# Kernel optimization log

Hardware: AMD Instinct MI355X
Metric: run time of the kernel (lower is better)

Reference implementation:

```python
import jax, jax.numpy as jnp
import numpy as np

N, E, B = 50000, 800000, 512
DIN, H, A, BT = 128, 256, 40, 5


def _ln(h, g, b):
    m = jnp.mean(h, -1, keepdims=True)
    v = jnp.mean((h - m) ** 2, -1, keepdims=True)
    return (h - m) * jax.lax.rsqrt(v + 1e-5) * g + b


def _gcn(x, w, b, src, dst, n):
    # PyG GCNConv: add self-loops, symmetric D^-1/2 (A+I) D^-1/2 normalization
    h = x @ w
    loop = jnp.arange(n)
    s = jnp.concatenate([src, loop])
    d = jnp.concatenate([dst, loop])
    deg = jax.ops.segment_sum(jnp.ones(s.shape[0], h.dtype), d, num_segments=n)
    dinv = jax.lax.rsqrt(jnp.maximum(deg, 1.0))
    coef = (dinv[s] * dinv[d])[:, None]
    return jax.ops.segment_sum(coef * h[s], d, num_segments=n) + b


def _mlp2(x, w1, b1, w2, b2):
    return jax.nn.relu(x @ w1 + b1) @ w2 + b2


def _mlp3(x, w1, b1, w2, b2, w3, b3):
    h = jax.nn.relu(x @ w1 + b1)
    h = jax.nn.relu(h @ w2 + b2)
    return h @ w3 + b3


def setup_inputs() -> dict:
    key = jax.random.key(0)
    ks = iter(jax.random.split(key, 64))
    p = lambda shape: jax.random.normal(next(ks), shape, jnp.float32) * 0.05
    inp = {}
    inp["x"] = jax.random.normal(next(ks), (N, DIN), jnp.float32)
    inp["edge_index"] = jax.random.randint(next(ks), (2, E), 0, N)
    inp["batch"] = jnp.sort(jax.random.randint(next(ks), (N,), 0, B))
    inp["new_node_indices"] = jax.random.randint(next(ks), (B,), 0, N)
    inp["focus_node_indices"] = jax.random.randint(next(ks), (B,), 0, N)
    inp["num_graphs"] = B
    inp["conv_w0"] = p((DIN, H)); inp["conv_b0"] = p((H,))
    inp["conv_w1"] = p((H, H)); inp["conv_b1"] = p((H,))
    inp["conv_w2"] = p((H, H)); inp["conv_b2"] = p((H,))
    for i in range(3):
        inp[f"ln_g{i}"] = jnp.ones((H,), jnp.float32)
        inp[f"ln_b{i}"] = jnp.zeros((H,), jnp.float32)
    inp["res_w0"] = p((DIN, H)); inp["res_b0"] = p((H,))
    inp["stop_w1"] = p((H, H)); inp["stop_b1"] = p((H,))
    inp["stop_w2"] = p((H, 1)); inp["stop_b2"] = p((1,))
    inp["addn_w1"] = p((H, H)); inp["addn_b1"] = p((H,))
    inp["addn_w2"] = p((H, A)); inp["addn_b2"] = p((A,))
    inp["addb_w1"] = p((H, H)); inp["addb_b1"] = p((H,))
    inp["addb_w2"] = p((H, BT)); inp["addb_b2"] = p((BT,))
    inp["edge_w1"] = p((2 * H, H)); inp["edge_b1"] = p((H,))
    inp["edge_w2"] = p((H, H // 2)); inp["edge_b2"] = p((H // 2,))
    inp["edge_w3"] = p((H // 2, 1)); inp["edge_b3"] = p((1,))
    inp["bond_w1"] = p((2 * H, H)); inp["bond_b1"] = p((H,))
    inp["bond_w2"] = p((H, H // 2)); inp["bond_b2"] = p((H // 2,))
    inp["bond_w3"] = p((H // 2, BT)); inp["bond_b3"] = p((BT,))
    return inp


def reference(x, edge_index, batch, new_node_indices, focus_node_indices, num_graphs,
              conv_w0, conv_b0, conv_w1, conv_b1, conv_w2, conv_b2,
              ln_g0, ln_b0, ln_g1, ln_b1, ln_g2, ln_b2,
              res_w0, res_b0,
              stop_w1, stop_b1, stop_w2, stop_b2,
              addn_w1, addn_b1, addn_w2, addn_b2,
              addb_w1, addb_b1, addb_w2, addb_b2,
              edge_w1, edge_b1, edge_w2, edge_b2, edge_w3, edge_b3,
              bond_w1, bond_b1, bond_w2, bond_b2, bond_w3, bond_b3):
    n = x.shape[0]
    src, dst = edge_index[0], edge_index[1]
    conv_params = [(conv_w0, conv_b0), (conv_w1, conv_b1), (conv_w2, conv_b2)]
    ln_params = [(ln_g0, ln_b0), (ln_g1, ln_b1), (ln_g2, ln_b2)]
    h = x
    for i in range(3):
        h_in = h
        cw, cb = conv_params[i]
        lg, lb = ln_params[i]
        h = _gcn(h, cw, cb, src, dst, n)
        h = jax.nn.relu(_ln(h, lg, lb))  # dropout: eval mode (identity)
        res = h_in @ res_w0 + res_b0 if i == 0 else h_in
        h = h + res
    node_embeddings = h  # [N, H]
    # global mean pool over graphs
    counts = jax.ops.segment_sum(jnp.ones(n, h.dtype), batch, num_segments=num_graphs)
    graph_embedding = jax.ops.segment_sum(node_embeddings, batch, num_segments=num_graphs) / jnp.maximum(counts, 1.0)[:, None]
    stop_logits = _mlp2(graph_embedding, stop_w1, stop_b1, stop_w2, stop_b2)
    add_node_logits = _mlp2(graph_embedding, addn_w1, addn_b1, addn_w2, addn_b2)
    add_bond_logits = _mlp2(node_embeddings[focus_node_indices], addb_w1, addb_b1, addb_w2, addb_b2)
    # pair each node with its graph's newly added node
    new_node_embeddings = node_embeddings[new_node_indices]  # [B, H]
    pair = jnp.concatenate([node_embeddings, new_node_embeddings[batch]], axis=1)  # [N, 2H]
    edge_selection_logits = _mlp3(pair, edge_w1, edge_b1, edge_w2, edge_b2, edge_w3, edge_b3)
    bond_type_logits = _mlp3(pair, bond_w1, bond_b1, bond_w2, bond_b2, bond_w3, bond_b3)
    return (stop_logits, add_node_logits, add_bond_logits, node_embeddings,
            edge_selection_logits, bond_type_logits)
```

## Files before the change

### kernel.cpp

```cpp
#include <hip/hip_runtime.h>

typedef short bf16x8 __attribute__((ext_vector_type(8)));
typedef float f32x4 __attribute__((ext_vector_type(4)));
typedef unsigned short u16;
typedef u16 u16x8 __attribute__((ext_vector_type(8)));

__device__ __forceinline__ float bf2f(u16 u) {
  union { float f; unsigned int i; } x; x.i = ((unsigned int)u) << 16; return x.f;
}
__device__ __forceinline__ u16 f2bf(float f) {
  union { float f; unsigned int i; } x; x.f = f;
  unsigned int r = x.i + 0x7fffu + ((x.i >> 16) & 1u);
  return (u16)(r >> 16);
}
__device__ __forceinline__ void st_out_(void* out, size_t idx, float v, int f32) {
  if (f32) ((float*)out)[idx] = v;
  else ((u16*)out)[idx] = f2bf(v);
}

__global__ void k_detect(const u16* __restrict__ xx, int* flag) {
  int j = threadIdx.x;
  u16 u = xx[2 * j];
  int ex = (u >> 7) & 0xFF;
  int insane = (u != 0) && (ex < 100 || ex > 140);
  unsigned long long m = __ballot(insane);
  if (j == 0) flag[0] = (__popcll(m) > 8) ? 1 : 0;
}

__global__ void k_cvt_big(const void* __restrict__ src, u16* __restrict__ dst, int n,
                          const int* __restrict__ flag) {
  int i = blockIdx.x * 256 + threadIdx.x;
  if (i >= n) return;
  dst[i] = (*flag) ? f2bf(((const float*)src)[i]) : ((const u16*)src)[i];
}

#define NSEG 38
struct Cvt { const void* src[NSEG]; int off[NSEG + 1]; };
__global__ void k_cvt_all(Cvt c, u16* __restrict__ dst, int total, const int* __restrict__ flag) {
  int i = blockIdx.x * 256 + threadIdx.x;
  if (i >= total) return;
  int s = 0;
  #pragma unroll 1
  while (i >= c.off[s + 1]) s++;
  int j = i - c.off[s];
  dst[i] = (*flag) ? f2bf(((const float*)c.src[s])[j]) : ((const u16*)c.src[s])[j];
}

__global__ void k_padbias(const u16* __restrict__ rb, u16* cbz) {
  int i = blockIdx.x * 256 + threadIdx.x;
  if (i < 512) cbz[i] = (i < 256) ? (u16)0 : rb[i - 256];
}

struct Tr { const u16* src[8]; u16* dst[8]; int lk[8]; int nc[8]; int off[9]; };
__global__ void k_tr_all(Tr c, int total) {
  int i = blockIdx.x * 256 + threadIdx.x;
  if (i >= total) return;
  int s = 0;
  #pragma unroll 1
  while (i >= c.off[s + 1]) s++;
  int j = i - c.off[s];
  int K = 1 << c.lk[s];
  int nrow = j >> c.lk[s], k = j & (K - 1);
  c.dst[s][j] = c.src[s][k * c.nc[s] + nrow];
}

__global__ void k_init(int* deg, int* cursor, int n) {
  int i = blockIdx.x * 256 + threadIdx.x;
  if (i < n) { deg[i] = 1; cursor[i] = 0; }
}
__global__ void k_deg(const int* __restrict__ dst, int* deg, int e) {
  int i = blockIdx.x * 256 + threadIdx.x;
  if (i < e) atomicAdd(&deg[dst[i]], 1);
}
__global__ void k_dinv(const int* __restrict__ deg, float* dinv, int n) {
  int i = blockIdx.x * 256 + threadIdx.x;
  if (i < n) dinv[i] = rsqrtf((float)deg[i]);
}
#define SCB 4096
__global__ __launch_bounds__(256) void k_scanA(const int* __restrict__ deg, int* bsum, int n) {
  int b = blockIdx.x, t = threadIdx.x;
  int base = b * SCB;
  int s = 0;
  for (int j = t; j < SCB; j += 256) { int i = base + j; s += (i < n) ? deg[i] - 1 : 0; }
  int l = t & 63, wid = t >> 6;
  #pragma unroll
  for (int o = 32; o; o >>= 1) s += __shfl_xor(s, o);
  __shared__ int red[4];
  if (l == 0) red[wid] = s;
  __syncthreads();
  if (t == 0) bsum[b] = red[0] + red[1] + red[2] + red[3];
}
__global__ void k_scanB(int* bsum, int nb, int* off, int n) {
  if (threadIdx.x == 0) {
    int c = 0;
    for (int i = 0; i < nb; i++) { int v = bsum[i]; bsum[i] = c; c += v; }
    off[n] = c;
  }
}
__global__ __launch_bounds__(256) void k_scanC(const int* __restrict__ deg, const int* __restrict__ bsum,
                                               int* off, int n) {
  int b = blockIdx.x, t = threadIdx.x;
  int base = b * SCB + t * 16;
  int loc[16]; int s = 0;
  #pragma unroll
  for (int j = 0; j < 16; j++) { int i = base + j; loc[j] = s; s += (i < n) ? deg[i] - 1 : 0; }
  int l = t & 63, wid = t >> 6;
  int incl = s;
  #pragma unroll
  for (int o = 1; o < 64; o <<= 1) { int y = __shfl_up(incl, o); if (l >= o) incl += y; }
  int excl = incl - s;
  __shared__ int ws[4];
  if (l == 63) ws[wid] = incl;
  __syncthreads();
  int woff = 0;
  for (int w = 0; w < wid; w++) woff += ws[w];
  int pre = bsum[b] + woff + excl;
  #pragma unroll
  for (int j = 0; j < 16; j++) { int i = base + j; if (i < n) off[i] = pre + loc[j]; }
}
__global__ void k_csr(const int* __restrict__ src, const int* __restrict__ dst,
                      const int* __restrict__ off, int* cursor, int* csr_src, int e) {
  int i = blockIdx.x * 256 + threadIdx.x;
  if (i >= e) return;
  int d = dst[i], s = src[i];
  int slot = atomicAdd(&cursor[d], 1);
  csr_src[off[d] + slot] = s;
}

template <int EPI, int K>
__global__ __launch_bounds__(512) void gemm_p(
    const u16* __restrict__ A, int lda,
    const u16* __restrict__ Bt,
    u16* __restrict__ C, int ldc,
    int M, int NC,
    const u16* __restrict__ colbias,
    const float* __restrict__ rowbias, int rbld, const int* __restrict__ rowmap) {
  __shared__ u16 Bs[64 * K];
  __shared__ u16 As[8 * 4 * 512];
  const int t = threadIdx.x;
  const int n0 = blockIdx.x * 64;
  const int m0 = blockIdx.y * 512;
  {
    const int ng = K >> 3;
    const int tot = 64 * ng;
    for (int i = t; i < tot; i += 512) {
      int c = i / ng, g = i - c * ng;
      u16x8 v = *reinterpret_cast<const u16x8*>(Bt + (size_t)(n0 + c) * K + g * 8);
      *reinterpret_cast<u16x8*>(&Bs[c * K + (g ^ (c & 7)) * 8]) = v;
    }
  }
  __syncthreads();

  const int wid = t >> 6, l = t & 63;
  const int rbase = m0 + wid * 64;
  const int lr = l & 15, lg = l >> 4;
  u16* Aw = &As[wid * 2048];
  const int srow = l >> 2;
  const int sg = (l & 3) ^ (srow & 3);

  auto stage = [&](int s) {
    int mi = s & 3, kk = s >> 2;
    int row = rbase + mi * 16 + srow;
    if (row >= M) row = M - 1;
    __builtin_amdgcn_global_load_lds(
        (const __attribute__((address_space(1))) unsigned int*)(A + (size_t)row * lda + kk * 32 + sg * 8),
        (__attribute__((address_space(3))) unsigned int*)(Aw + (s & 3) * 512), 16, 0, 0);
  };

  f32x4 acc[4][4] = {};
  bf16x8 bfr[4];
  const int S = K >> 3;
  stage(0); stage(1); stage(2);
  #pragma unroll
  for (int s = 0; s < S; s++) {
    const int buf = s & 3, mi = s & 3, kk = s >> 2;
    __builtin_amdgcn_sched_barrier(0);
    if (s + 3 < S) stage(s + 3);
    const int rem = (s + 3 < S) ? 3 : (S - 1 - s);
    if (rem >= 3)      asm volatile("s_waitcnt vmcnt(3)" ::: "memory");
    else if (rem == 2) asm volatile("s_waitcnt vmcnt(2)" ::: "memory");
    else if (rem == 1) asm volatile("s_waitcnt vmcnt(1)" ::: "memory");
    else               asm volatile("s_waitcnt vmcnt(0)" ::: "memory");
    __builtin_amdgcn_sched_barrier(0);
    if (mi == 0) {
      #pragma unroll
      for (int ni = 0; ni < 4; ni++) {
        int g = kk * 4 + lg;
        bfr[ni] = *reinterpret_cast<const bf16x8*>(&Bs[(ni * 16 + lr) * K + (g ^ (lr & 7)) * 8]);
      }
    }
    const u16* Ab = Aw + buf * 512;
    bf16x8 af = *reinterpret_cast<const bf16x8*>(&Ab[lr * 32 + (lg ^ (lr & 3)) * 8]);
    #pragma unroll
    for (int ni = 0; ni < 4; ni++)
      acc[mi][ni] = __builtin_amdgcn_mfma_f32_16x16x32_bf16(af, bfr[ni], acc[mi][ni], 0, 0, 0);
  }

  #pragma unroll
  for (int mi = 0; mi < 4; mi++) {
    int rowi[4];
    #pragma unroll
    for (int r = 0; r < 4; r++) rowi[r] = rbase + mi * 16 + lg * 4 + r;
    float rbv[4][4];
    if (EPI == 3) {
      int rmv[4];
      #pragma unroll
      for (int r = 0; r < 4; r++) {
        int rr = rowi[r]; if (rr >= M) rr = M - 1;
        rmv[r] = rowmap[rr];
      }
      #pragma unroll
      for (int ni = 0; ni < 4; ni++)
        #pragma unroll
        for (int r = 0; r < 4; r++)
          rbv[ni][r] = rowbias[(size_t)rmv[r] * rbld + n0 + ni * 16 + lr];
    }
    #pragma unroll
    for (int ni = 0; ni < 4; ni++) {
      int col = n0 + ni * 16 + lr;
      float cbv = 0.f;
      if (EPI == 1 || EPI == 2) cbv = bf2f(colbias[col]);
      #pragma unroll
      for (int r = 0; r < 4; r++) {
        if (rowi[r] < M) {
          float v = acc[mi][ni][r];
          if (EPI == 1 || EPI == 2) v += cbv;
          if (EPI == 3) v += rbv[ni][r];
          if (EPI == 2 || EPI == 3) v = fmaxf(v, 0.f);
          C[(size_t)rowi[r] * ldc + col] = f2bf(v);
        }
      }
    }
  }
}

__global__ __launch_bounds__(256, 6) void k_agg(
    const u16* __restrict__ hw, int hwld, const u16* __restrict__ cb,
    const u16* __restrict__ lng, const u16* __restrict__ lnb,
    const u16* __restrict__ res, int resld, const float* __restrict__ dinv,
    const int* __restrict__ off, const int* __restrict__ csr_src,
    u16* __restrict__ hout, int n) {
  int l = threadIdx.x & 63;
  int v = blockIdx.x * 4 + (threadIdx.x >> 6);
  if (v >= n) return;
  const int half = l >> 5;
  const int c0 = (l & 31) * 8;
  float a[8] = {0, 0, 0, 0, 0, 0, 0, 0};
  int s = off[v], e = off[v + 1];
  int i = s;
  for (; i + 7 < e; i += 8) {
    int u0 = csr_src[i + half],     u1 = csr_src[i + 2 + half];
    int u2 = csr_src[i + 4 + half], u3 = csr_src[i + 6 + half];
    float w0 = dinv[u0], w1 = dinv[u1], w2 = dinv[u2], w3 = dinv[u3];
    u16x8 r0 = *reinterpret_cast<const u16x8*>(hw + (size_t)u0 * hwld + c0);
    u16x8 r1 = *reinterpret_cast<const u16x8*>(hw + (size_t)u1 * hwld + c0);
    u16x8 r2 = *reinterpret_cast<const u16x8*>(hw + (size_t)u2 * hwld + c0);
    u16x8 r3 = *reinterpret_cast<const u16x8*>(hw + (size_t)u3 * hwld + c0);
    #pragma unroll
    for (int j = 0; j < 8; j++)
      a[j] += w0 * bf2f(r0[j]) + w1 * bf2f(r1[j]) + w2 * bf2f(r2[j]) + w3 * bf2f(r3[j]);
  }
  for (; i < e; i += 2) {
    int idx = i + half;
    if (idx < e) {
      int u = csr_src[idx];
      float w = dinv[u];
      u16x8 r = *reinterpret_cast<const u16x8*>(hw + (size_t)u * hwld + c0);
      #pragma unroll
      for (int j = 0; j < 8; j++) a[j] += w * bf2f(r[j]);
    }
  }
  #pragma unroll
  for (int j = 0; j < 8; j++) a[j] += __shfl_xor(a[j], 32);
  float dv = dinv[v];
  u16x8 sv = *reinterpret_cast<const u16x8*>(hw + (size_t)v * hwld + c0);
  u16x8 cbv = *reinterpret_cast<const u16x8*>(cb + c0);
  float sum = 0.f;
  #pragma unroll
  for (int j = 0; j < 8; j++) {
    a[j] = dv * (dv * bf2f(sv[j]) + a[j]) + bf2f(cbv[j]);
    sum += a[j];
  }
  #pragma unroll
  for (int o = 16; o; o >>= 1) sum += __shfl_xor(sum, o);
  float mean = sum * (1.f / 256.f);
  float vs = 0.f;
  #pragma unroll
  for (int j = 0; j < 8; j++) { float d = a[j] - mean; vs += d * d; }
  #pragma unroll
  for (int o = 16; o; o >>= 1) vs += __shfl_xor(vs, o);
  float rs = rsqrtf(vs * (1.f / 256.f) + 1e-5f);
  u16x8 gv = *reinterpret_cast<const u16x8*>(lng + c0);
  u16x8 bv = *reinterpret_cast<const u16x8*>(lnb + c0);
  u16x8 rv = *reinterpret_cast<const u16x8*>(res + (size_t)v * resld + c0);
  u16x8 ov;
  #pragma unroll
  for (int j = 0; j < 8; j++)
    ov[j] = f2bf(fmaxf((a[j] - mean) * rs * bf2f(gv[j]) + bf2f(bv[j]), 0.f) + bf2f(rv[j]));
  if (half == 0)
    *reinterpret_cast<u16x8*>(hout + (size_t)v * 256 + c0) = ov;
}

__global__ __launch_bounds__(256) void k_pool(const u16* __restrict__ h, const int* __restrict__ batch,
                                              int n, float* gemb) {
  int g = blockIdx.x, c = threadIdx.x;
  int lo = 0, hi = n;
  while (lo < hi) { int mid = (lo + hi) >> 1; if (batch[mid] < g) lo = mid + 1; else hi = mid; }
  int s = lo;
  lo = s; hi = n;
  while (lo < hi) { int mid = (lo + hi) >> 1; if (batch[mid] < g + 1) lo = mid + 1; else hi = mid; }
  int e = lo;
  float a0 = 0.f, a1 = 0.f, a2 = 0.f, a3 = 0.f;
  int i = s;
  for (; i + 3 < e; i += 4) {
    a0 += bf2f(h[(size_t)i * 256 + c]);
    a1 += bf2f(h[(size_t)(i + 1) * 256 + c]);
    a2 += bf2f(h[(size_t)(i + 2) * 256 + c]);
    a3 += bf2f(h[(size_t)(i + 3) * 256 + c]);
  }
  for (; i < e; i++) a0 += bf2f(h[(size_t)i * 256 + c]);
  float acc = (a0 + a1) + (a2 + a3);
  int cnt = e - s; if (cnt < 1) cnt = 1;
  gemb[g * 256 + c] = acc / (float)cnt;
}

__global__ __launch_bounds__(256) void k_glin(const u16* __restrict__ h, const int* __restrict__ nidx,
                                              const u16* __restrict__ W, const u16* __restrict__ b1,
                                              float* g1, int ld, int ofs) {
  int b = blockIdx.x, t = threadIdx.x;
  __shared__ float sin_[256];
  sin_[t] = bf2f(h[(size_t)nidx[b] * 256 + t]);
  __syncthreads();
  float acc = bf2f(b1[t]);
  #pragma unroll 8
  for (int k = 0; k < 256; k++) acc += sin_[k] * bf2f(W[k * 256 + t]);
  g1[(size_t)b * ld + ofs + t] = acc;
}

template <int OUTD>
__global__ __launch_bounds__(256) void k_mlp2(const float* __restrict__ inf32,
                                              const u16* __restrict__ inbf, const int* __restrict__ idx,
                                              const u16* __restrict__ W1, const u16* __restrict__ b1,
                                              const u16* __restrict__ W2, const u16* __restrict__ b2,
                                              void* __restrict__ out, size_t obase,
                                              const int* __restrict__ flag) {
  int b = blockIdx.x, t = threadIdx.x;
  __shared__ float sin_[256];
  __shared__ float sh[256];
  sin_[t] = inf32 ? inf32[b * 256 + t] : bf2f(inbf[(size_t)idx[b] * 256 + t]);
  __syncthreads();
  float acc = bf2f(b1[t]);
  #pragma unroll 8
  for (int k = 0; k < 256; k++) acc += sin_[k] * bf2f(W1[k * 256 + t]);
  sh[t] = fmaxf(acc, 0.f);
  __syncthreads();
  if (t < OUTD) {
    float a2 = bf2f(b2[t]);
    #pragma unroll 8
    for (int k = 0; k < 256; k++) a2 += sh[k] * bf2f(W2[k * OUTD + t]);
    st_out_(out, obase + (size_t)b * OUTD + t, a2, *flag);
  }
}

__global__ __launch_bounds__(256) void k_final(const u16* __restrict__ t2e, const u16* __restrict__ t2b,
                                               const u16* __restrict__ w3e, const u16* __restrict__ b3e,
                                               const u16* __restrict__ w3b, const u16* __restrict__ b3b,
                                               void* __restrict__ out, size_t oe, size_t ob, int M,
                                               const int* __restrict__ flag) {
  int r = blockIdx.x * 4 + (threadIdx.x >> 6);
  int l = threadIdx.x & 63;
  if (r >= M) return;
  float p[6] = {0, 0, 0, 0, 0, 0};
  #pragma unroll
  for (int j = 0; j < 2; j++) {
    int k = l * 2 + j;
    float te = bf2f(t2e[(size_t)r * 128 + k]);
    float tb = bf2f(t2b[(size_t)r * 128 + k]);
    p[0] += te * bf2f(w3e[k]);
    #pragma unroll
    for (int q = 0; q < 5; q++) p[1 + q] += tb * bf2f(w3b[k * 5 + q]);
  }
  #pragma unroll
  for (int q = 0; q < 6; q++)
    #pragma unroll
    for (int o = 32; o; o >>= 1) p[q] += __shfl_xor(p[q], o);
  if (l == 0) {
    int f32 = *flag;
    st_out_(out, oe + r, p[0] + bf2f(b3e[0]), f32);
    #pragma unroll
    for (int q = 0; q < 5; q++)
      st_out_(out, ob + (size_t)r * 5 + q, p[1 + q] + bf2f(b3b[q]), f32);
  }
}

__global__ void k_emit8(const u16* __restrict__ src, void* __restrict__ out, size_t obase, int n8,
                        const int* __restrict__ flag) {
  int i = blockIdx.x * 256 + threadIdx.x;
  if (i >= n8) return;
  u16x8 v = reinterpret_cast<const u16x8*>(src)[i];
  if (*flag) {
    float4* fo = (float4*)((float*)out + obase);
    float4 lo, hi;
    lo.x = bf2f(v[0]); lo.y = bf2f(v[1]); lo.z = bf2f(v[2]); lo.w = bf2f(v[3]);
    hi.x = bf2f(v[4]); hi.y = bf2f(v[5]); hi.z = bf2f(v[6]); hi.w = bf2f(v[7]);
    fo[(size_t)i * 2] = lo; fo[(size_t)i * 2 + 1] = hi;
  } else {
    reinterpret_cast<u16x8*>((u16*)out + obase)[i] = v;
  }
}

extern "C" void kernel_launch(void* const* d_in, const int* in_sizes, int n_in,
                              void* d_out, int out_size, void* d_ws, size_t ws_size,
                              hipStream_t stream) {
  const int N = in_sizes[0] / 128;
  const int E = in_sizes[1] / 2;
  const int B = in_sizes[3];

  const int* ei    = (const int*)d_in[1];
  const int* srcp  = ei;
  const int* dstp  = ei + E;
  const int* batch = (const int*)d_in[2];
  const int* newi  = (const int*)d_in[3];
  const int* focus = (const int*)d_in[4];

  const size_t o_stop = 0;
  const size_t o_addn = (size_t)B;
  const size_t o_addb = (size_t)B + (size_t)B * 40;
  const size_t o_emb  = o_addb + (size_t)B * 5;
  const size_t o_esel = o_emb + (size_t)N * 256;
  const size_t o_bond = o_esel + (size_t)N;

  char* p = (char*)d_ws;
  auto alloc = [&](size_t bytes) -> void* {
    void* r = (void*)p;
    p += (bytes + 255) & ~(size_t)255;
    return r;
  };
  int* flag = (int*)alloc(4);
  static const int seg_din[NSEG] = {6,7,8,9,10,11, 12,13,14,15,16,17, 18,19,
                                    20,21,22,23, 24,25,26,27, 28,29,30,31,
                                    32,33,34,35,36,37, 38,39,40,41,42,43};
  static const int seg_len[NSEG] = {32768,256,65536,256,65536,256, 256,256,256,256,256,256,
                                    32768,256, 65536,256,256,1, 65536,256,10240,40,
                                    65536,256,1280,5, 131072,256,32768,128,128,1,
                                    131072,256,32768,128,640,5};
  int wtotal = 0;
  int seg_off[NSEG + 1];
  for (int i = 0; i < NSEG; i++) { seg_off[i] = wtotal; wtotal += seg_len[i]; }
  seg_off[NSEG] = wtotal;
  u16* wbf = (u16*)alloc((size_t)wtotal * 2);
  u16* wt_f0  = (u16*)alloc(512 * 128 * 2);
  u16* wt_cw1 = (u16*)alloc(256 * 256 * 2);
  u16* wt_cw2 = (u16*)alloc(256 * 256 * 2);
  u16* wt_t1  = (u16*)alloc(512 * 256 * 2);
  u16* wt_e2  = (u16*)alloc(128 * 256 * 2);
  u16* wt_b2  = (u16*)alloc(128 * 256 * 2);
  u16* cbz    = (u16*)alloc(512 * 2);
  int*   deg     = (int*)alloc((size_t)N * 4);
  int*   cursor  = (int*)alloc((size_t)N * 4);
  int*   off     = (int*)alloc((size_t)(N + 1) * 4);
  float* dinv    = (float*)alloc((size_t)N * 4);
  int*   bsum    = (int*)alloc(64 * 4);
  float* gemb    = (float*)alloc((size_t)B * 256 * 4);
  float* g1full  = (float*)alloc((size_t)B * 512 * 4);
  int*   csr_src = (int*)alloc((size_t)E * 4);
  u16*   xbf     = (u16*)alloc((size_t)N * 128 * 2);
  u16*   P1      = (u16*)alloc((size_t)N * 256 * 2);
  u16*   P2      = (u16*)alloc((size_t)N * 256 * 2);
  u16*   P3      = (u16*)alloc((size_t)N * 256 * 2);

  auto wseg = [&](int i) -> u16* { return wbf + seg_off[i]; };
  u16 *cw0 = wseg(0), *cb0 = wseg(1), *cw1 = wseg(2), *cb1 = wseg(3), *cw2 = wseg(4), *cb2 = wseg(5);
  u16 *lg0 = wseg(6), *lb0 = wseg(7), *lg1 = wseg(8), *lb1 = wseg(9), *lg2 = wseg(10), *lb2 = wseg(11);
  u16 *rw0 = wseg(12), *rb0 = wseg(13);
  u16 *sw1 = wseg(14), *sb1 = wseg(15), *sw2 = wseg(16), *sb2 = wseg(17);
  u16 *aw1 = wseg(18), *ab1 = wseg(19), *aw2 = wseg(20), *ab2 = wseg(21);
  u16 *bw1 = wseg(22), *bb1 = wseg(23), *bw2 = wseg(24), *bb2 = wseg(25);
  u16 *ew1 = wseg(26), *eb1 = wseg(27), *ew2 = wseg(28), *eb2 = wseg(29), *ew3 = wseg(30), *eb3 = wseg(31);
  u16 *qw1 = wseg(32), *qb1 = wseg(33), *qw2 = wseg(34), *qb2 = wseg(35), *qw3 = wseg(36), *qb3 = wseg(37);

  k_detect<<<1, 64, 0, stream>>>((const u16*)d_in[0], flag);
  k_cvt_big<<<(N * 128 + 255) / 256, 256, 0, stream>>>(d_in[0], xbf, N * 128, flag);
  Cvt cd;
  for (int i = 0; i < NSEG; i++) cd.src[i] = d_in[seg_din[i]];
  for (int i = 0; i <= NSEG; i++) cd.off[i] = seg_off[i];
  k_cvt_all<<<(wtotal + 255) / 256, 256, 0, stream>>>(cd, wbf, wtotal, flag);
  k_padbias<<<2, 256, 0, stream>>>(rb0, cbz);

  const int NB = (N + 255) / 256;
  const int EBk = (E + 255) / 256;
  const int NBS = (N + SCB - 1) / SCB;

  k_init<<<NB, 256, 0, stream>>>(deg, cursor, N);
  k_deg<<<EBk, 256, 0, stream>>>(dstp, deg, E);
  k_dinv<<<NB, 256, 0, stream>>>(deg, dinv, N);
  k_scanA<<<NBS, 256, 0, stream>>>(deg, bsum, N);
  k_scanB<<<1, 64, 0, stream>>>(bsum, NBS, off, N);
  k_scanC<<<NBS, 256, 0, stream>>>(deg, bsum, off, N);
  k_csr<<<EBk, 256, 0, stream>>>(srcp, dstp, off, cursor, csr_src, E);

  {
    Tr td;
    const u16* ts[8] = {cw0, rw0, cw1, cw2, ew1, qw1, ew2, qw2};
    u16* tdst[8] = {wt_f0, wt_f0 + 256 * 128, wt_cw1, wt_cw2, wt_t1, wt_t1 + 256 * 256, wt_e2, wt_b2};
    int tlk[8] = {7, 7, 8, 8, 8, 8, 8, 8};
    int tnc[8] = {256, 256, 256, 256, 256, 256, 128, 128};
    int tlen[8] = {32768, 32768, 65536, 65536, 65536, 65536, 32768, 32768};
    int tot = 0;
    for (int i = 0; i < 8; i++) {
      td.src[i] = ts[i]; td.dst[i] = tdst[i]; td.lk[i] = tlk[i]; td.nc[i] = tnc[i];
      td.off[i] = tot; tot += tlen[i];
    }
    td.off[8] = tot;
    k_tr_all<<<(tot + 255) / 256, 256, 0, stream>>>(td, tot);
  }

  const int MB5 = (N + 511) / 512;
  const int AGB = (N + 3) / 4;
  u16* PF = P1;

  gemm_p<1, 128><<<dim3(8, MB5), 512, 0, stream>>>(xbf, 128, wt_f0, PF, 512, N, 512, cbz, nullptr, 0, nullptr);
  k_agg<<<AGB, 256, 0, stream>>>(PF, 512, cb0, lg0, lb0, PF + 256, 512, dinv, off, csr_src, P3, N);
  gemm_p<0, 256><<<dim3(4, MB5), 512, 0, stream>>>(P3, 256, wt_cw1, P1, 256, N, 256, nullptr, nullptr, 0, nullptr);
  k_agg<<<AGB, 256, 0, stream>>>(P1, 256, cb1, lg1, lb1, P3, 256, dinv, off, csr_src, P2, N);
  gemm_p<0, 256><<<dim3(4, MB5), 512, 0, stream>>>(P2, 256, wt_cw2, P1, 256, N, 256, nullptr, nullptr, 0, nullptr);
  k_agg<<<AGB, 256, 0, stream>>>(P1, 256, cb2, lg2, lb2, P2, 256, dinv, off, csr_src, P3, N);

  k_emit8<<<(N * 256 / 8 + 255) / 256, 256, 0, stream>>>(P3, d_out, o_emb, N * 256 / 8, flag);

  k_pool<<<B, 256, 0, stream>>>(P3, batch, N, gemb);
  k_glin<<<B, 256, 0, stream>>>(P3, newi, ew1 + 256 * 256, eb1, g1full, 512, 0);
  k_glin<<<B, 256, 0, stream>>>(P3, newi, qw1 + 256 * 256, qb1, g1full, 512, 256);
  k_mlp2<1><<<B, 256, 0, stream>>>(gemb, nullptr, nullptr, sw1, sb1, sw2, sb2, d_out, o_stop, flag);
  k_mlp2<40><<<B, 256, 0, stream>>>(gemb, nullptr, nullptr, aw1, ab1, aw2, ab2, d_out, o_addn, flag);
  k_mlp2<5><<<B, 256, 0, stream>>>(nullptr, P3, focus, bw1, bb1, bw2, bb2, d_out, o_addb, flag);

  u16* T1 = PF;
  gemm_p<3, 256><<<dim3(8, MB5), 512, 0, stream>>>(P3, 256, wt_t1, T1, 512, N, 512, nullptr, g1full, 512, batch);
  u16* t2e = P3;
  u16* t2b = P3 + (size_t)N * 128;
  gemm_p<2, 256><<<dim3(2, MB5), 512, 0, stream>>>(T1, 512, wt_e2, t2e, 128, N, 128, eb2, nullptr, 0, nullptr);
  gemm_p<2, 256><<<dim3(2, MB5), 512, 0, stream>>>(T1 + 256, 512, wt_b2, t2b, 128, N, 128, qb2, nullptr, 0, nullptr);
  k_final<<<(N + 3) / 4, 256, 0, stream>>>(t2e, t2b, ew3, eb3, qw3, qb3, d_out, o_esel, o_bond, N, flag);
}
```

Before: 615.2 us.

## Precompute edge weights in CSR, fuse embedding emit, swap GEMM grid order

The CSR build now stores dinv[src] per edge, so aggregation reads a contiguous weight array instead of doing a dependent random gather into dinv. The final aggregation kernel writes the node embeddings straight to the output buffer, which removes the separate k_emit8 pass over N×256 values. GEMM launches now put M tiles on grid x, padded to a multiple of 8 with an early-exit guard, likely for better L2 reuse or XCD distribution of the shared B tiles. k_agg launch bounds are raised to allow more waves per SIMD. The cost is an extra E-sized float array plus its write, and possible register pressure in k_agg.

```diff
diff --git a/kernel.cpp b/kernel.cpp
--- a/kernel.cpp
+++ b/kernel.cpp
@@ -119,12 +119,15 @@
   for (int j = 0; j < 16; j++) { int i = base + j; if (i < n) off[i] = pre + loc[j]; }
 }
 __global__ void k_csr(const int* __restrict__ src, const int* __restrict__ dst,
-                      const int* __restrict__ off, int* cursor, int* csr_src, int e) {
+                      const float* __restrict__ dinv, const int* __restrict__ off,
+                      int* cursor, int* csr_src, float* csr_w, int e) {
   int i = blockIdx.x * 256 + threadIdx.x;
   if (i >= e) return;
   int d = dst[i], s = src[i];
   int slot = atomicAdd(&cursor[d], 1);
-  csr_src[off[d] + slot] = s;
+  int pos = off[d] + slot;
+  csr_src[pos] = s;
+  csr_w[pos] = dinv[s];
 }
 
 template <int EPI, int K>
@@ -138,8 +141,9 @@
   __shared__ u16 Bs[64 * K];
   __shared__ u16 As[8 * 4 * 512];
   const int t = threadIdx.x;
-  const int n0 = blockIdx.x * 64;
-  const int m0 = blockIdx.y * 512;
+  const int m0 = blockIdx.x * 512;
+  const int n0 = blockIdx.y * 64;
+  if (m0 >= M) return;
   {
     const int ng = K >> 3;
     const int tot = 64 * ng;
@@ -234,12 +238,14 @@
   }
 }
 
-__global__ __launch_bounds__(256, 6) void k_agg(
+__global__ __launch_bounds__(256, 8) void k_agg(
     const u16* __restrict__ hw, int hwld, const u16* __restrict__ cb,
     const u16* __restrict__ lng, const u16* __restrict__ lnb,
     const u16* __restrict__ res, int resld, const float* __restrict__ dinv,
     const int* __restrict__ off, const int* __restrict__ csr_src,
-    u16* __restrict__ hout, int n) {
+    const float* __restrict__ csr_w,
+    u16* __restrict__ hout, int n,
+    void* __restrict__ out2, size_t obase, const int* __restrict__ flag) {
   int l = threadIdx.x & 63;
   int v = blockIdx.x * 4 + (threadIdx.x >> 6);
   if (v >= n) return;
@@ -251,7 +257,8 @@
   for (; i + 7 < e; i += 8) {
     int u0 = csr_src[i + half],     u1 = csr_src[i + 2 + half];
     int u2 = csr_src[i + 4 + half], u3 = csr_src[i + 6 + half];
-    float w0 = dinv[u0], w1 = dinv[u1], w2 = dinv[u2], w3 = dinv[u3];
+    float w0 = csr_w[i + half],     w1 = csr_w[i + 2 + half];
+    float w2 = csr_w[i + 4 + half], w3 = csr_w[i + 6 + half];
     u16x8 r0 = *reinterpret_cast<const u16x8*>(hw + (size_t)u0 * hwld + c0);
     u16x8 r1 = *reinterpret_cast<const u16x8*>(hw + (size_t)u1 * hwld + c0);
     u16x8 r2 = *reinterpret_cast<const u16x8*>(hw + (size_t)u2 * hwld + c0);
@@ -264,7 +271,7 @@
     int idx = i + half;
     if (idx < e) {
       int u = csr_src[idx];
-      float w = dinv[u];
+      float w = csr_w[idx];
       u16x8 r = *reinterpret_cast<const u16x8*>(hw + (size_t)u * hwld + c0);
       #pragma unroll
       for (int j = 0; j < 8; j++) a[j] += w * bf2f(r[j]);
@@ -293,12 +300,28 @@
   u16x8 gv = *reinterpret_cast<const u16x8*>(lng + c0);
   u16x8 bv = *reinterpret_cast<const u16x8*>(lnb + c0);
   u16x8 rv = *reinterpret_cast<const u16x8*>(res + (size_t)v * resld + c0);
+  float y[8];
   u16x8 ov;
   #pragma unroll
-  for (int j = 0; j < 8; j++)
-    ov[j] = f2bf(fmaxf((a[j] - mean) * rs * bf2f(gv[j]) + bf2f(bv[j]), 0.f) + bf2f(rv[j]));
-  if (half == 0)
+  for (int j = 0; j < 8; j++) {
+    y[j] = fmaxf((a[j] - mean) * rs * bf2f(gv[j]) + bf2f(bv[j]), 0.f) + bf2f(rv[j]);
+    ov[j] = f2bf(y[j]);
+  }
+  if (half == 0) {
     *reinterpret_cast<u16x8*>(hout + (size_t)v * 256 + c0) = ov;
+    if (out2) {
+      if (*flag) {
+        float4 lo, hi;
+        lo.x = bf2f(ov[0]); lo.y = bf2f(ov[1]); lo.z = bf2f(ov[2]); lo.w = bf2f(ov[3]);
+        hi.x = bf2f(ov[4]); hi.y = bf2f(ov[5]); hi.z = bf2f(ov[6]); hi.w = bf2f(ov[7]);
+        float* fo = (float*)out2 + obase + (size_t)v * 256 + c0;
+        *reinterpret_cast<float4*>(fo) = lo;
+        *reinterpret_cast<float4*>(fo + 4) = hi;
+      } else {
+        *reinterpret_cast<u16x8*>((u16*)out2 + obase + (size_t)v * 256 + c0) = ov;
+      }
+    }
+  }
 }
 
 __global__ __launch_bounds__(256) void k_pool(const u16* __restrict__ h, const int* __restrict__ batch,
@@ -390,22 +413,6 @@
     #pragma unroll
     for (int q = 0; q < 5; q++)
       st_out_(out, ob + (size_t)r * 5 + q, p[1 + q] + bf2f(b3b[q]), f32);
-  }
-}
-
-__global__ void k_emit8(const u16* __restrict__ src, void* __restrict__ out, size_t obase, int n8,
-                        const int* __restrict__ flag) {
-  int i = blockIdx.x * 256 + threadIdx.x;
-  if (i >= n8) return;
-  u16x8 v = reinterpret_cast<const u16x8*>(src)[i];
-  if (*flag) {
-    float4* fo = (float4*)((float*)out + obase);
-    float4 lo, hi;
-    lo.x = bf2f(v[0]); lo.y = bf2f(v[1]); lo.z = bf2f(v[2]); lo.w = bf2f(v[3]);
-    hi.x = bf2f(v[4]); hi.y = bf2f(v[5]); hi.z = bf2f(v[6]); hi.w = bf2f(v[7]);
-    fo[(size_t)i * 2] = lo; fo[(size_t)i * 2 + 1] = hi;
-  } else {
-    reinterpret_cast<u16x8*>((u16*)out + obase)[i] = v;
   }
 }
 
@@ -464,6 +471,7 @@
   float* gemb    = (float*)alloc((size_t)B * 256 * 4);
   float* g1full  = (float*)alloc((size_t)B * 512 * 4);
   int*   csr_src = (int*)alloc((size_t)E * 4);
+  float* csr_w   = (float*)alloc((size_t)E * 4);
   u16*   xbf     = (u16*)alloc((size_t)N * 128 * 2);
   u16*   P1      = (u16*)alloc((size_t)N * 256 * 2);
   u16*   P2      = (u16*)alloc((size_t)N * 256 * 2);
@@ -497,7 +505,7 @@
   k_scanA<<<NBS, 256, 0, stream>>>(deg, bsum, N);
   k_scanB<<<1, 64, 0, stream>>>(bsum, NBS, off, N);
   k_scanC<<<NBS, 256, 0, stream>>>(deg, bsum, off, N);
-  k_csr<<<EBk, 256, 0, stream>>>(srcp, dstp, off, cursor, csr_src, E);
+  k_csr<<<EBk, 256, 0, stream>>>(srcp, dstp, dinv, off, cursor, csr_src, csr_w, E);
 
   {
     Tr td;
@@ -516,17 +524,16 @@
   }
 
   const int MB5 = (N + 511) / 512;
+  const int MBP = (MB5 + 7) & ~7;
   const int AGB = (N + 3) / 4;
   u16* PF = P1;
 
-  gemm_p<1, 128><<<dim3(8, MB5), 512, 0, stream>>>(xbf, 128, wt_f0, PF, 512, N, 512, cbz, nullptr, 0, nullptr);
-  k_agg<<<AGB, 256, 0, stream>>>(PF, 512, cb0, lg0, lb0, PF + 256, 512, dinv, off, csr_src, P3, N);
-  gemm_p<0, 256><<<dim3(4, MB5), 512, 0, stream>>>(P3, 256, wt_cw1, P1, 256, N, 256, nullptr, nullptr, 0, nullptr);
-  k_agg<<<AGB, 256, 0, stream>>>(P1, 256, cb1, lg1, lb1, P3, 256, dinv, off, csr_src, P2, N);
-  gemm_p<0, 256><<<dim3(4, MB5), 512, 0, stream>>>(P2, 256, wt_cw2, P1, 256, N, 256, nullptr, nullptr, 0, nullptr);
-  k_agg<<<AGB, 256, 0, stream>>>(P1, 256, cb2, lg2, lb2, P2, 256, dinv, off, csr_src, P3, N);
-
-  k_emit8<<<(N * 256 / 8 + 255) / 256, 256, 0, stream>>>(P3, d_out, o_emb, N * 256 / 8, flag);
+  gemm_p<1, 128><<<dim3(MBP, 8), 512, 0, stream>>>(xbf, 128, wt_f0, PF, 512, N, 512, cbz, nullptr, 0, nullptr);
+  k_agg<<<AGB, 256, 0, stream>>>(PF, 512, cb0, lg0, lb0, PF + 256, 512, dinv, off, csr_src, csr_w, P3, N, nullptr, 0, flag);
+  gemm_p<0, 256><<<dim3(MBP, 4), 512, 0, stream>>>(P3, 256, wt_cw1, P1, 256, N, 256, nullptr, nullptr, 0, nullptr);
+  k_agg<<<AGB, 256, 0, stream>>>(P1, 256, cb1, lg1, lb1, P3, 256, dinv, off, csr_src, csr_w, P2, N, nullptr, 0, flag);
+  gemm_p<0, 256><<<dim3(MBP, 4), 512, 0, stream>>>(P2, 256, wt_cw2, P1, 256, N, 256, nullptr, nullptr, 0, nullptr);
+  k_agg<<<AGB, 256, 0, stream>>>(P1, 256, cb2, lg2, lb2, P2, 256, dinv, off, csr_src, csr_w, P3, N, d_out, o_emb, flag);
 
   k_pool<<<B, 256, 0, stream>>>(P3, batch, N, gemb);
   k_glin<<<B, 256, 0, stream>>>(P3, newi, ew1 + 256 * 256, eb1, g1full, 512, 0);
@@ -536,10 +543,10 @@
   k_mlp2<5><<<B, 256, 0, stream>>>(nullptr, P3, focus, bw1, bb1, bw2, bb2, d_out, o_addb, flag);
 
   u16* T1 = PF;
-  gemm_p<3, 256><<<dim3(8, MB5), 512, 0, stream>>>(P3, 256, wt_t1, T1, 512, N, 512, nullptr, g1full, 512, batch);
+  gemm_p<3, 256><<<dim3(MBP, 8), 512, 0, stream>>>(P3, 256, wt_t1, T1, 512, N, 512, nullptr, g1full, 512, batch);
   u16* t2e = P3;
   u16* t2b = P3 + (size_t)N * 128;
-  gemm_p<2, 256><<<dim3(2, MB5), 512, 0, stream>>>(T1, 512, wt_e2, t2e, 128, N, 128, eb2, nullptr, 0, nullptr);
-  gemm_p<2, 256><<<dim3(2, MB5), 512, 0, stream>>>(T1 + 256, 512, wt_b2, t2b, 128, N, 128, qb2, nullptr, 0, nullptr);
+  gemm_p<2, 256><<<dim3(MBP, 2), 512, 0, stream>>>(T1, 512, wt_e2, t2e, 128, N, 128, eb2, nullptr, 0, nullptr);
+  gemm_p<2, 256><<<dim3(MBP, 2), 512, 0, stream>>>(T1 + 256, 512, wt_b2, t2b, 128, N, 128, qb2, nullptr, 0, nullptr);
   k_final<<<(N + 3) / 4, 256, 0, stream>>>(t2e, t2b, ew3, eb3, qw3, qb3, d_out, o_esel, o_bond, N, flag);
 }
```

Measured after the change: 584.8 us. -4.9%, faster.
